# Optimization experiments

Hardware: AMD Instinct MI355X
Metric: run time of the kernel (lower is better)

The kernel has to match this reference:

```python
import jax, jax.numpy as jnp
import numpy as np

F, N, D, K = 32, 4096, 64, 512
COMMITMENT_COST = 0.25


def setup_inputs() -> dict:
    key = jax.random.key(0)
    k1, k2 = jax.random.split(key)
    inputs = jax.random.normal(k1, (F, N, D), dtype=jnp.float32)
    # GlorotUniform on weight shape [F, D, K]
    limit = float(np.sqrt(6.0 / (D + K)))
    w = jax.random.uniform(k2, (F, D, K), dtype=jnp.float32, minval=-limit, maxval=limit)
    return {"inputs": inputs, "w": w}


def reference(inputs, w):
    # inputs: [F, N, D], w: [F, D, K]
    distances = (
        jnp.sum(inputs ** 2, axis=2, keepdims=True)
        - 2.0 * jnp.einsum('fnd,fdk->fnk', inputs, w)
        + jnp.sum(w ** 2, axis=1, keepdims=True)
    )
    enc_idx = jnp.argmin(distances, axis=2)  # [F, N]
    w_t = jnp.swapaxes(w, 1, 2)  # [F, K, D]
    quantized = jnp.take_along_axis(w_t, enc_idx[:, :, None], axis=1)  # [F, N, D]
    e_latent_loss = jnp.mean((jax.lax.stop_gradient(quantized) - inputs) ** 2)
    q_latent_loss = jnp.mean((quantized - jax.lax.stop_gradient(inputs)) ** 2)
    loss = q_latent_loss + COMMITMENT_COST * e_latent_loss
    # straight-through estimator
    output = inputs + jax.lax.stop_gradient(quantized - inputs)
    return output, loss
```

## Files before the change

kernel.cpp:

```cpp
#include <hip/hip_runtime.h>
#include <math.h>

#define NF 32
#define NN 4096
#define ND 64
#define NK 512

#define LOSS_SCALE (1.25f / (float)(NF * NN * ND))
#define TAU 3e-4f

#define NPARTIAL (NF * NN * 4 / 256)

typedef short bf16x8 __attribute__((ext_vector_type(8)));
typedef float f32x4 __attribute__((ext_vector_type(4)));

static __device__ __forceinline__ unsigned short f2bf_rne(float f) {
    unsigned int u = __float_as_uint(f);
    u += 0x7FFFu + ((u >> 16) & 1u);
    return (unsigned short)(u >> 16);
}
static __device__ __forceinline__ float bf2f(unsigned short h) {
    return __uint_as_float(((unsigned int)h) << 16);
}

static __device__ __forceinline__ void gload_lds16(const void* g, void* l) {
    __builtin_amdgcn_global_load_lds(
        (const __attribute__((address_space(1))) unsigned int*)g,
        (__attribute__((address_space(3))) unsigned int*)l, 16, 0, 0);
}

__global__ __launch_bounds__(256)
void vq_prep_w(const float* __restrict__ w, float* __restrict__ wt,
               unsigned short* __restrict__ wh, unsigned short* __restrict__ wl,
               float* __restrict__ w2h) {
    const int gid = blockIdx.x * 256 + threadIdx.x;
    const int dc = gid & 7;
    const int k  = (gid >> 3) & (NK - 1);
    const int f  = gid >> 12;
    const float* __restrict__ wf = w + (size_t)f * ND * NK;
    const size_t rowo = ((size_t)f * NK + k) * ND + dc * 8;

    float v[8];
    unsigned short hh[8], ll[8];
    float s = 0.0f;
#pragma unroll
    for (int j = 0; j < 8; ++j) {
        v[j] = wf[(dc * 8 + j) * NK + k];
        s = fmaf(v[j], v[j], s);
        hh[j] = f2bf_rne(v[j]);
        ll[j] = f2bf_rne(v[j] - bf2f(hh[j]));
    }
    *(float4*)(wt + rowo)     = make_float4(v[0], v[1], v[2], v[3]);
    *(float4*)(wt + rowo + 4) = make_float4(v[4], v[5], v[6], v[7]);
    *(ushort4*)(wh + rowo)     = make_ushort4(hh[0], hh[1], hh[2], hh[3]);
    *(ushort4*)(wh + rowo + 4) = make_ushort4(hh[4], hh[5], hh[6], hh[7]);
    *(ushort4*)(wl + rowo)     = make_ushort4(ll[0], ll[1], ll[2], ll[3]);
    *(ushort4*)(wl + rowo + 4) = make_ushort4(ll[4], ll[5], ll[6], ll[7]);

    s += __shfl_xor(s, 1, 64);
    s += __shfl_xor(s, 2, 64);
    s += __shfl_xor(s, 4, 64);
    if (dc == 0) w2h[f * NK + k] = 0.5f * s;
}

__global__ __launch_bounds__(256, 4)
void vq_argmin(const float* __restrict__ x_in,
               const unsigned short* __restrict__ wh,
               const unsigned short* __restrict__ wl,
               const float* __restrict__ w2h,
               unsigned int* __restrict__ keys,
               unsigned char* __restrict__ flags) {
    const int b    = blockIdx.x;
    const int j    = b >> 3;
    const int f    = (b & 7) * 4 + (j & 3);
    const int xt   = j >> 2;
    const int tid  = threadIdx.x;
    const int wave = tid >> 6;
    const int lane = tid & 63;
    const int lc   = lane & 15;
    const int q    = lane >> 4;
    const int n0   = xt * 128 + wave * 32;

    __shared__ float w2s[NK];
    __shared__ __align__(16) unsigned short bstage[2][4096];

    for (int t = tid; t < NK; t += 256) w2s[t] = w2h[f * NK + t];

    bf16x8 ah[2][2], al[2][2];
    const float* __restrict__ xbase = x_in + ((size_t)f * NN + n0 + lc) * ND;
#pragma unroll
    for (int mt = 0; mt < 2; ++mt) {
#pragma unroll
        for (int s = 0; s < 2; ++s) {
            const float* p = xbase + mt * 16 * ND + s * 32 + q * 8;
            float4 u0 = *(const float4*)(p);
            float4 u1 = *(const float4*)(p + 4);
            float xv[8] = {-u0.x, -u0.y, -u0.z, -u0.w, -u1.x, -u1.y, -u1.z, -u1.w};
            bf16x8 h, l;
#pragma unroll
            for (int jj = 0; jj < 8; ++jj) {
                unsigned short hb = f2bf_rne(xv[jj]);
                unsigned short lb = f2bf_rne(xv[jj] - bf2f(hb));
                h[jj] = (short)hb;
                l[jj] = (short)lb;
            }
            ah[mt][s] = h;
            al[mt][s] = l;
        }
    }

    const unsigned short* __restrict__ whf = wh + (size_t)f * NK * ND;
    const unsigned short* __restrict__ wlf = wl + (size_t)f * NK * ND;

    float m1[8], m2[8], kmin[8];
#pragma unroll
    for (int ri = 0; ri < 8; ++ri) { m1[ri] = INFINITY; m2[ri] = INFINITY; kmin[ri] = INFINITY; }

#define STAGE(st, pb) do {                                                  \
    _Pragma("unroll")                                                       \
    for (int rep = 0; rep < 2; ++rep) {                                     \
        const int c  = wave * 2 + rep;                                      \
        const int tl = c >> 2;                                              \
        const int sg = (c >> 1) & 1;                                        \
        const unsigned short* src = ((c & 1) ? wlf : whf) +                 \
            (size_t)((st) * 32 + tl * 16 + lc) * ND + q * 8 + sg * 32;      \
        gload_lds16(src, &bstage[pb][c * 512]);                             \
    }                                                                       \
} while (0)

    STAGE(0, 0);

    for (int st = 0; st < 16; ++st) {
        __syncthreads();
        if (st < 15) STAGE(st + 1, (st + 1) & 1);
        const unsigned short* __restrict__ bb = &bstage[st & 1][0];

#pragma unroll
        for (int tl = 0; tl < 2; ++tl) {
            const int col = st * 32 + tl * 16 + lc;
            bf16x8 bh0 = *(const bf16x8*)(bb + (tl * 4 + 0) * 512 + lane * 8);
            bf16x8 bl0 = *(const bf16x8*)(bb + (tl * 4 + 1) * 512 + lane * 8);
            bf16x8 bh1 = *(const bf16x8*)(bb + (tl * 4 + 2) * 512 + lane * 8);
            bf16x8 bl1 = *(const bf16x8*)(bb + (tl * 4 + 3) * 512 + lane * 8);
            const float w2 = w2s[col];
#pragma unroll
            for (int mt = 0; mt < 2; ++mt) {
                f32x4 c = {w2, w2, w2, w2};
                c = __builtin_amdgcn_mfma_f32_16x16x32_bf16(ah[mt][0], bh0, c, 0, 0, 0);
                c = __builtin_amdgcn_mfma_f32_16x16x32_bf16(ah[mt][1], bh1, c, 0, 0, 0);
                c = __builtin_amdgcn_mfma_f32_16x16x32_bf16(ah[mt][0], bl0, c, 0, 0, 0);
                c = __builtin_amdgcn_mfma_f32_16x16x32_bf16(ah[mt][1], bl1, c, 0, 0, 0);
                c = __builtin_amdgcn_mfma_f32_16x16x32_bf16(al[mt][0], bh0, c, 0, 0, 0);
                c = __builtin_amdgcn_mfma_f32_16x16x32_bf16(al[mt][1], bh1, c, 0, 0, 0);
                c = __builtin_amdgcn_mfma_f32_16x16x32_bf16(al[mt][0], bl0, c, 0, 0, 0);
                c = __builtin_amdgcn_mfma_f32_16x16x32_bf16(al[mt][1], bl1, c, 0, 0, 0);
#pragma unroll
                for (int r = 0; r < 4; ++r) {
                    const int ri = mt * 4 + r;
                    const float sc = c[r];
                    const float key = __uint_as_float(
                        (__float_as_uint(sc) & 0xFFFFFE00u) | (unsigned int)col);
                    kmin[ri] = fminf(kmin[ri], key);
                    m2[ri] = __builtin_amdgcn_fmed3f(sc, m1[ri], m2[ri]);
                    m1[ri] = fminf(sc, m1[ri]);
                }
            }
        }
    }

#pragma unroll
    for (int ri = 0; ri < 8; ++ri) {
        float a1 = m1[ri], a2 = m2[ri], ak = kmin[ri];
#pragma unroll
        for (int off = 1; off < 16; off <<= 1) {
            const float b1 = __shfl_xor(a1, off, 64);
            const float b2 = __shfl_xor(a2, off, 64);
            const float bk = __shfl_xor(ak, off, 64);
            a2 = fminf(fminf(a2, b2), fmaxf(a1, b1));
            a1 = fminf(a1, b1);
            ak = fminf(ak, bk);
        }
        m1[ri] = a1; m2[ri] = a2; kmin[ri] = ak;
    }

    if (lc == 0) {
#pragma unroll
        for (int mt = 0; mt < 2; ++mt) {
            const int g = f * NN + n0 + mt * 16 + q * 4;
            uint4 kv;
            uchar4 fl;
#pragma unroll
            for (int r = 0; r < 4; ++r) {
                const int ri = mt * 4 + r;
                ((unsigned int*)&kv)[r] = __float_as_uint(kmin[ri]) & 0x1FFu;
                ((unsigned char*)&fl)[r] = (m2[ri] - m1[ri] < TAU) ? 1 : 0;
            }
            *(uint4*)(keys + g) = kv;
            *(uchar4*)(flags + g) = fl;
        }
    }
}

__global__ __launch_bounds__(256)
void vq_rescue(const float* __restrict__ x_in, const float* __restrict__ wt,
               const float* __restrict__ w2h,
               const unsigned char* __restrict__ flags,
               unsigned int* __restrict__ keys) {
    const int lane = threadIdx.x & 63;
    const int wid  = (blockIdx.x * 256 + threadIdx.x) >> 6;
    const int base = wid * 16;

    const unsigned char flv = flags[base + (lane & 15)];
    unsigned long long m = __ballot(flv != 0 && lane < 16);
    while (m) {
        const int r = __ffsll(m) - 1;
        m &= m - 1;
        const int g = base + r;
        const int f = g >> 12;
        const float* __restrict__ xr  = x_in + (size_t)g * ND;
        const float* __restrict__ wtf = wt + (size_t)f * NK * ND;
        unsigned long long best = 0xFFFFFFFFFFFFFFFFULL;
#pragma unroll 1
        for (int jj = 0; jj < 8; ++jj) {
            const int col = jj * 64 + lane;
            const float* __restrict__ wr = wtf + (size_t)col * ND;
            float t = w2h[f * NK + col];
#pragma unroll
            for (int d = 0; d < ND; d += 4) {
                float4 xv = *(const float4*)(xr + d);
                float4 wv = *(const float4*)(wr + d);
                t = fmaf(-xv.x, wv.x, t);
                t = fmaf(-xv.y, wv.y, t);
                t = fmaf(-xv.z, wv.z, t);
                t = fmaf(-xv.w, wv.w, t);
            }
            unsigned int u = __float_as_uint(t);
            u ^= (unsigned int)((int)u >> 31) | 0x80000000u;
            const unsigned long long key =
                ((unsigned long long)u << 32) | (unsigned int)col;
            best = key < best ? key : best;
        }
#pragma unroll
        for (int off = 32; off > 0; off >>= 1) {
            const unsigned long long o = __shfl_xor(best, off, 64);
            best = o < best ? o : best;
        }
        if (lane == 0) keys[g] = (unsigned int)(best & 0xFFFFFFFFULL);
    }
}

__global__ __launch_bounds__(256)
void vq_gather(const float* __restrict__ x_in, const float* __restrict__ wt,
               const unsigned int* __restrict__ keys, float* __restrict__ out,
               float* __restrict__ partial) {
    const int gid = blockIdx.x * 256 + threadIdx.x;
    const int row = gid >> 2;
    const int c   = (gid & 3) * 16;
    const int f   = row >> 12;
    const unsigned int k = keys[row];

    const float* __restrict__ q16 = wt + ((size_t)f * NK + k) * ND + c;
    const float* __restrict__ x16 = x_in + (size_t)row * ND + c;
    float* __restrict__ o16       = out + (size_t)row * ND + c;

    float lsum = 0.0f;
#pragma unroll
    for (int jj = 0; jj < 4; ++jj) {
        float4 qv = *(const float4*)(q16 + 4 * jj);
        float4 xv = *(const float4*)(x16 + 4 * jj);
        const float dx0 = qv.x - xv.x;
        const float dx1 = qv.y - xv.y;
        const float dx2 = qv.z - xv.z;
        const float dx3 = qv.w - xv.w;
        lsum = fmaf(dx0, dx0, lsum);
        lsum = fmaf(dx1, dx1, lsum);
        lsum = fmaf(dx2, dx2, lsum);
        lsum = fmaf(dx3, dx3, lsum);
        *(float4*)(o16 + 4 * jj) = qv;
    }

#pragma unroll
    for (int off = 32; off > 0; off >>= 1) {
        lsum += __shfl_down(lsum, off, 64);
    }
    __shared__ float wsum[4];
    if ((threadIdx.x & 63) == 0) wsum[threadIdx.x >> 6] = lsum;
    __syncthreads();
    if (threadIdx.x == 0) {
        partial[blockIdx.x] = wsum[0] + wsum[1] + wsum[2] + wsum[3];
    }
}

__global__ __launch_bounds__(256)
void vq_loss_final(const float* __restrict__ partial, float* __restrict__ loss) {
    float s = 0.0f;
    for (int i = threadIdx.x; i < NPARTIAL; i += 256) s += partial[i];
#pragma unroll
    for (int off = 32; off > 0; off >>= 1) s += __shfl_down(s, off, 64);
    __shared__ float wsum[4];
    if ((threadIdx.x & 63) == 0) wsum[threadIdx.x >> 6] = s;
    __syncthreads();
    if (threadIdx.x == 0) {
        *loss = (wsum[0] + wsum[1] + wsum[2] + wsum[3]) * LOSS_SCALE;
    }
}

extern "C" void kernel_launch(void* const* d_in, const int* in_sizes, int n_in,
                              void* d_out, int out_size, void* d_ws, size_t ws_size,
                              hipStream_t stream) {
    const float* x_in = (const float*)d_in[0];
    const float* w    = (const float*)d_in[1];
    float* out        = (float*)d_out;

    float* wt  = (float*)d_ws;
    float* w2h = wt + (size_t)NF * NK * ND;
    unsigned short* wh = (unsigned short*)(w2h + NF * NK);
    unsigned short* wl = wh + (size_t)NF * NK * ND;
    unsigned int* keys = (unsigned int*)(wl + (size_t)NF * NK * ND);
    unsigned char* flags = (unsigned char*)(keys + (size_t)NF * NN);
    float* partial = (float*)(flags + (size_t)NF * NN);

    float* loss_slot = out + (size_t)NF * NN * ND;

    vq_prep_w<<<NF * NK * 8 / 256, 256, 0, stream>>>(w, wt, wh, wl, w2h);

    vq_argmin<<<NF * NN / 128, 256, 0, stream>>>(x_in, wh, wl, w2h, keys, flags);

    vq_rescue<<<NF * NN / 16 / 4, 256, 0, stream>>>(x_in, wt, w2h, flags, keys);

    vq_gather<<<NF * NN * 4 / 256, 256, 0, stream>>>(x_in, wt, keys, out, partial);

    vq_loss_final<<<1, 256, 0, stream>>>(partial, loss_slot);
}
```

Measured before the change: 165.4 us.

## Fuse rescue, gather and loss into argmin kernel; drop low-low MFMA term

The rescue pass, the gather/loss pass and the final reduction are folded into the argmin kernel. Keys and flags now stay in LDS, near-tie rows are recomputed exactly per wave, and each block writes its output rows and atomically adds its loss share into a slot that prep_w zeroes. The weight prep kernel now transposes through LDS so its global reads are coalesced. The bf16 low×low correction MFMAs are removed, which cuts MFMA work by a quarter but slightly weakens the accuracy of the split-bf16 distance, leaning more on the fp32 rescue path. It also replaces three launches and the key/partial round trips through global memory, at the cost of a nondeterministic atomic loss sum.

```diff
diff --git a/kernel.cpp b/kernel.cpp
--- a/kernel.cpp
+++ b/kernel.cpp
@@ -9,8 +9,6 @@
 #define LOSS_SCALE (1.25f / (float)(NF * NN * ND))
 #define TAU 3e-4f
 
-#define NPARTIAL (NF * NN * 4 / 256)
-
 typedef short bf16x8 __attribute__((ext_vector_type(8)));
 typedef float f32x4 __attribute__((ext_vector_type(4)));
 
@@ -32,44 +30,67 @@
 __global__ __launch_bounds__(256)
 void vq_prep_w(const float* __restrict__ w, float* __restrict__ wt,
                unsigned short* __restrict__ wh, unsigned short* __restrict__ wl,
-               float* __restrict__ w2h) {
-    const int gid = blockIdx.x * 256 + threadIdx.x;
-    const int dc = gid & 7;
-    const int k  = (gid >> 3) & (NK - 1);
-    const int f  = gid >> 12;
+               float* __restrict__ w2h, float* __restrict__ loss_slot) {
+    __shared__ float lds[64 * 65];
+    const int t  = threadIdx.x;
+    const int f  = blockIdx.x >> 3;
+    const int k0 = (blockIdx.x & 7) * 64;
     const float* __restrict__ wf = w + (size_t)f * ND * NK;
-    const size_t rowo = ((size_t)f * NK + k) * ND + dc * 8;
-
-    float v[8];
-    unsigned short hh[8], ll[8];
+
+    if (blockIdx.x == 0 && t == 0) *loss_slot = 0.0f;
+
+    {
+        const int d = t >> 2, qq = t & 3;
+#pragma unroll
+        for (int i = 0; i < 4; ++i) {
+            const int c4 = qq + i * 4;
+            const float4 v = *(const float4*)(wf + (size_t)d * NK + k0 + c4 * 4);
+            lds[d * 65 + c4 * 4 + 0] = v.x;
+            lds[d * 65 + c4 * 4 + 1] = v.y;
+            lds[d * 65 + c4 * 4 + 2] = v.z;
+            lds[d * 65 + c4 * 4 + 3] = v.w;
+        }
+    }
+    __syncthreads();
+
+    const int k = t >> 2, p = t & 3;
+    float v[16];
     float s = 0.0f;
 #pragma unroll
-    for (int j = 0; j < 8; ++j) {
-        v[j] = wf[(dc * 8 + j) * NK + k];
+    for (int j = 0; j < 16; ++j) {
+        v[j] = lds[(p * 16 + j) * 65 + k];
         s = fmaf(v[j], v[j], s);
+    }
+    s += __shfl_xor(s, 1, 64);
+    s += __shfl_xor(s, 2, 64);
+    if (p == 0) w2h[f * NK + k0 + k] = 0.5f * s;
+
+    const size_t rowo = ((size_t)f * NK + k0 + k) * ND + p * 16;
+    unsigned short hh[16], ll[16];
+#pragma unroll
+    for (int j = 0; j < 16; ++j) {
         hh[j] = f2bf_rne(v[j]);
         ll[j] = f2bf_rne(v[j] - bf2f(hh[j]));
     }
-    *(float4*)(wt + rowo)     = make_float4(v[0], v[1], v[2], v[3]);
-    *(float4*)(wt + rowo + 4) = make_float4(v[4], v[5], v[6], v[7]);
-    *(ushort4*)(wh + rowo)     = make_ushort4(hh[0], hh[1], hh[2], hh[3]);
-    *(ushort4*)(wh + rowo + 4) = make_ushort4(hh[4], hh[5], hh[6], hh[7]);
-    *(ushort4*)(wl + rowo)     = make_ushort4(ll[0], ll[1], ll[2], ll[3]);
-    *(ushort4*)(wl + rowo + 4) = make_ushort4(ll[4], ll[5], ll[6], ll[7]);
-
-    s += __shfl_xor(s, 1, 64);
-    s += __shfl_xor(s, 2, 64);
-    s += __shfl_xor(s, 4, 64);
-    if (dc == 0) w2h[f * NK + k] = 0.5f * s;
+#pragma unroll
+    for (int i = 0; i < 4; ++i) {
+        *(float4*)(wt + rowo + i * 4) =
+            make_float4(v[i*4+0], v[i*4+1], v[i*4+2], v[i*4+3]);
+        *(ushort4*)(wh + rowo + i * 4) =
+            make_ushort4(hh[i*4+0], hh[i*4+1], hh[i*4+2], hh[i*4+3]);
+        *(ushort4*)(wl + rowo + i * 4) =
+            make_ushort4(ll[i*4+0], ll[i*4+1], ll[i*4+2], ll[i*4+3]);
+    }
 }
 
 __global__ __launch_bounds__(256, 4)
 void vq_argmin(const float* __restrict__ x_in,
                const unsigned short* __restrict__ wh,
                const unsigned short* __restrict__ wl,
+               const float* __restrict__ wt,
                const float* __restrict__ w2h,
-               unsigned int* __restrict__ keys,
-               unsigned char* __restrict__ flags) {
+               float* __restrict__ out,
+               float* __restrict__ loss_slot) {
     const int b    = blockIdx.x;
     const int j    = b >> 3;
     const int f    = (b & 7) * 4 + (j & 3);
@@ -80,9 +101,12 @@
     const int lc   = lane & 15;
     const int q    = lane >> 4;
     const int n0   = xt * 128 + wave * 32;
+    const int g0b  = f * NN + xt * 128;
 
     __shared__ float w2s[NK];
     __shared__ __align__(16) unsigned short bstage[2][4096];
+    __shared__ unsigned int lds_key[128];
+    __shared__ unsigned char lds_flag[128];
 
     for (int t = tid; t < NK; t += 256) w2s[t] = w2h[f * NK + t];
 
@@ -96,16 +120,16 @@
             float4 u0 = *(const float4*)(p);
             float4 u1 = *(const float4*)(p + 4);
             float xv[8] = {-u0.x, -u0.y, -u0.z, -u0.w, -u1.x, -u1.y, -u1.z, -u1.w};
-            bf16x8 h, l;
+            bf16x8 hh, ll;
 #pragma unroll
             for (int jj = 0; jj < 8; ++jj) {
                 unsigned short hb = f2bf_rne(xv[jj]);
                 unsigned short lb = f2bf_rne(xv[jj] - bf2f(hb));
-                h[jj] = (short)hb;
-                l[jj] = (short)lb;
-            }
-            ah[mt][s] = h;
-            al[mt][s] = l;
+                hh[jj] = (short)hb;
+                ll[jj] = (short)lb;
+            }
+            ah[mt][s] = hh;
+            al[mt][s] = ll;
         }
     }
 
@@ -152,8 +176,6 @@
                 c = __builtin_amdgcn_mfma_f32_16x16x32_bf16(ah[mt][1], bl1, c, 0, 0, 0);
                 c = __builtin_amdgcn_mfma_f32_16x16x32_bf16(al[mt][0], bh0, c, 0, 0, 0);
                 c = __builtin_amdgcn_mfma_f32_16x16x32_bf16(al[mt][1], bh1, c, 0, 0, 0);
-                c = __builtin_amdgcn_mfma_f32_16x16x32_bf16(al[mt][0], bl0, c, 0, 0, 0);
-                c = __builtin_amdgcn_mfma_f32_16x16x32_bf16(al[mt][1], bl1, c, 0, 0, 0);
 #pragma unroll
                 for (int r = 0; r < 4; ++r) {
                     const int ri = mt * 4 + r;
@@ -186,122 +208,94 @@
     if (lc == 0) {
 #pragma unroll
         for (int mt = 0; mt < 2; ++mt) {
-            const int g = f * NN + n0 + mt * 16 + q * 4;
-            uint4 kv;
-            uchar4 fl;
 #pragma unroll
             for (int r = 0; r < 4; ++r) {
                 const int ri = mt * 4 + r;
-                ((unsigned int*)&kv)[r] = __float_as_uint(kmin[ri]) & 0x1FFu;
-                ((unsigned char*)&fl)[r] = (m2[ri] - m1[ri] < TAU) ? 1 : 0;
-            }
-            *(uint4*)(keys + g) = kv;
-            *(uchar4*)(flags + g) = fl;
-        }
-    }
-}
-
-__global__ __launch_bounds__(256)
-void vq_rescue(const float* __restrict__ x_in, const float* __restrict__ wt,
-               const float* __restrict__ w2h,
-               const unsigned char* __restrict__ flags,
-               unsigned int* __restrict__ keys) {
-    const int lane = threadIdx.x & 63;
-    const int wid  = (blockIdx.x * 256 + threadIdx.x) >> 6;
-    const int base = wid * 16;
-
-    const unsigned char flv = flags[base + (lane & 15)];
-    unsigned long long m = __ballot(flv != 0 && lane < 16);
-    while (m) {
-        const int r = __ffsll(m) - 1;
-        m &= m - 1;
-        const int g = base + r;
-        const int f = g >> 12;
-        const float* __restrict__ xr  = x_in + (size_t)g * ND;
+                const int lr = wave * 32 + mt * 16 + q * 4 + r;
+                lds_key[lr]  = __float_as_uint(kmin[ri]) & 0x1FFu;
+                lds_flag[lr] = (m2[ri] - m1[ri] < TAU) ? 1 : 0;
+            }
+        }
+    }
+    __syncthreads();
+
+    {
+        const int lr32 = wave * 32 + (lane & 31);
+        const int fl = (lane < 32) ? lds_flag[lr32] : 0;
+        unsigned long long mm = __ballot(fl != 0);
         const float* __restrict__ wtf = wt + (size_t)f * NK * ND;
-        unsigned long long best = 0xFFFFFFFFFFFFFFFFULL;
+        while (mm) {
+            const int r = __ffsll(mm) - 1;
+            mm &= mm - 1;
+            const int grow = g0b + wave * 32 + r;
+            const float* __restrict__ xr = x_in + (size_t)grow * ND;
+            unsigned long long best = 0xFFFFFFFFFFFFFFFFULL;
 #pragma unroll 1
+            for (int jj = 0; jj < 8; ++jj) {
+                const int col = jj * 64 + lane;
+                const float* __restrict__ wr = wtf + (size_t)col * ND;
+                float t = w2s[col];
+#pragma unroll
+                for (int d = 0; d < ND; d += 4) {
+                    float4 xv = *(const float4*)(xr + d);
+                    float4 wv = *(const float4*)(wr + d);
+                    t = fmaf(-xv.x, wv.x, t);
+                    t = fmaf(-xv.y, wv.y, t);
+                    t = fmaf(-xv.z, wv.z, t);
+                    t = fmaf(-xv.w, wv.w, t);
+                }
+                unsigned int u = __float_as_uint(t);
+                u ^= (unsigned int)((int)u >> 31) | 0x80000000u;
+                const unsigned long long key =
+                    ((unsigned long long)u << 32) | (unsigned int)col;
+                best = key < best ? key : best;
+            }
+#pragma unroll
+            for (int off = 32; off > 0; off >>= 1) {
+                const unsigned long long o = __shfl_xor(best, off, 64);
+                best = o < best ? o : best;
+            }
+            if (lane == 0) lds_key[wave * 32 + r] = (unsigned int)(best & 0x1FFu);
+        }
+    }
+    __syncthreads();
+
+    {
+        const int row_l = tid >> 1;
+        const int part  = tid & 1;
+        const int grow  = g0b + row_l;
+        const unsigned int k = lds_key[row_l];
+        const float* __restrict__ q32 = wt + ((size_t)f * NK + k) * ND + part * 32;
+        const float* __restrict__ x32 = x_in + (size_t)grow * ND + part * 32;
+        float* __restrict__ o32       = out + (size_t)grow * ND + part * 32;
+
+        float lsum = 0.0f;
+#pragma unroll
         for (int jj = 0; jj < 8; ++jj) {
-            const int col = jj * 64 + lane;
-            const float* __restrict__ wr = wtf + (size_t)col * ND;
-            float t = w2h[f * NK + col];
-#pragma unroll
-            for (int d = 0; d < ND; d += 4) {
-                float4 xv = *(const float4*)(xr + d);
-                float4 wv = *(const float4*)(wr + d);
-                t = fmaf(-xv.x, wv.x, t);
-                t = fmaf(-xv.y, wv.y, t);
-                t = fmaf(-xv.z, wv.z, t);
-                t = fmaf(-xv.w, wv.w, t);
-            }
-            unsigned int u = __float_as_uint(t);
-            u ^= (unsigned int)((int)u >> 31) | 0x80000000u;
-            const unsigned long long key =
-                ((unsigned long long)u << 32) | (unsigned int)col;
-            best = key < best ? key : best;
-        }
+            float4 qv = *(const float4*)(q32 + 4 * jj);
+            float4 xv = *(const float4*)(x32 + 4 * jj);
+            const float dx0 = qv.x - xv.x;
+            const float dx1 = qv.y - xv.y;
+            const float dx2 = qv.z - xv.z;
+            const float dx3 = qv.w - xv.w;
+            lsum = fmaf(dx0, dx0, lsum);
+            lsum = fmaf(dx1, dx1, lsum);
+            lsum = fmaf(dx2, dx2, lsum);
+            lsum = fmaf(dx3, dx3, lsum);
+            *(float4*)(o32 + 4 * jj) = qv;
+        }
+
 #pragma unroll
         for (int off = 32; off > 0; off >>= 1) {
-            const unsigned long long o = __shfl_xor(best, off, 64);
-            best = o < best ? o : best;
-        }
-        if (lane == 0) keys[g] = (unsigned int)(best & 0xFFFFFFFFULL);
-    }
-}
-
-__global__ __launch_bounds__(256)
-void vq_gather(const float* __restrict__ x_in, const float* __restrict__ wt,
-               const unsigned int* __restrict__ keys, float* __restrict__ out,
-               float* __restrict__ partial) {
-    const int gid = blockIdx.x * 256 + threadIdx.x;
-    const int row = gid >> 2;
-    const int c   = (gid & 3) * 16;
-    const int f   = row >> 12;
-    const unsigned int k = keys[row];
-
-    const float* __restrict__ q16 = wt + ((size_t)f * NK + k) * ND + c;
-    const float* __restrict__ x16 = x_in + (size_t)row * ND + c;
-    float* __restrict__ o16       = out + (size_t)row * ND + c;
-
-    float lsum = 0.0f;
-#pragma unroll
-    for (int jj = 0; jj < 4; ++jj) {
-        float4 qv = *(const float4*)(q16 + 4 * jj);
-        float4 xv = *(const float4*)(x16 + 4 * jj);
-        const float dx0 = qv.x - xv.x;
-        const float dx1 = qv.y - xv.y;
-        const float dx2 = qv.z - xv.z;
-        const float dx3 = qv.w - xv.w;
-        lsum = fmaf(dx0, dx0, lsum);
-        lsum = fmaf(dx1, dx1, lsum);
-        lsum = fmaf(dx2, dx2, lsum);
-        lsum = fmaf(dx3, dx3, lsum);
-        *(float4*)(o16 + 4 * jj) = qv;
-    }
-
-#pragma unroll
-    for (int off = 32; off > 0; off >>= 1) {
-        lsum += __shfl_down(lsum, off, 64);
-    }
-    __shared__ float wsum[4];
-    if ((threadIdx.x & 63) == 0) wsum[threadIdx.x >> 6] = lsum;
-    __syncthreads();
-    if (threadIdx.x == 0) {
-        partial[blockIdx.x] = wsum[0] + wsum[1] + wsum[2] + wsum[3];
-    }
-}
-
-__global__ __launch_bounds__(256)
-void vq_loss_final(const float* __restrict__ partial, float* __restrict__ loss) {
-    float s = 0.0f;
-    for (int i = threadIdx.x; i < NPARTIAL; i += 256) s += partial[i];
-#pragma unroll
-    for (int off = 32; off > 0; off >>= 1) s += __shfl_down(s, off, 64);
-    __shared__ float wsum[4];
-    if ((threadIdx.x & 63) == 0) wsum[threadIdx.x >> 6] = s;
-    __syncthreads();
-    if (threadIdx.x == 0) {
-        *loss = (wsum[0] + wsum[1] + wsum[2] + wsum[3]) * LOSS_SCALE;
+            lsum += __shfl_down(lsum, off, 64);
+        }
+        __shared__ float wsum[4];
+        if ((tid & 63) == 0) wsum[tid >> 6] = lsum;
+        __syncthreads();
+        if (tid == 0) {
+            atomicAdd(loss_slot,
+                      (wsum[0] + wsum[1] + wsum[2] + wsum[3]) * LOSS_SCALE);
+        }
     }
 }
 
@@ -316,19 +310,11 @@
     float* w2h = wt + (size_t)NF * NK * ND;
     unsigned short* wh = (unsigned short*)(w2h + NF * NK);
     unsigned short* wl = wh + (size_t)NF * NK * ND;
-    unsigned int* keys = (unsigned int*)(wl + (size_t)NF * NK * ND);
-    unsigned char* flags = (unsigned char*)(keys + (size_t)NF * NN);
-    float* partial = (float*)(flags + (size_t)NF * NN);
 
     float* loss_slot = out + (size_t)NF * NN * ND;
 
-    vq_prep_w<<<NF * NK * 8 / 256, 256, 0, stream>>>(w, wt, wh, wl, w2h);
-
-    vq_argmin<<<NF * NN / 128, 256, 0, stream>>>(x_in, wh, wl, w2h, keys, flags);
-
-    vq_rescue<<<NF * NN / 16 / 4, 256, 0, stream>>>(x_in, wt, w2h, flags, keys);
-
-    vq_gather<<<NF * NN * 4 / 256, 256, 0, stream>>>(x_in, wt, keys, out, partial);
-
-    vq_loss_final<<<1, 256, 0, stream>>>(partial, loss_slot);
-}
+    vq_prep_w<<<NF * 8, 256, 0, stream>>>(w, wt, wh, wl, w2h, loss_slot);
+
+    vq_argmin<<<NF * NN / 128, 256, 0, stream>>>(x_in, wh, wl, wt, w2h,
+                                                 out, loss_slot);
+}
```

New measurement: 148.1 us. 10.5% less time.
